# Kernel optimization log

Measured on AMD Instinct MI355X. Metric: run time of the kernel, lower is better.

## Reference

```python
import jax, jax.numpy as jnp
import numpy as np

S = 8192        # total packed tokens
HID = 3072      # hidden_size
NHQ = 24        # query heads
NHKV = 8        # kv heads (GQA)
HD = 128        # head dim
NM = 2          # modalities (experts); tokens assumed modality-sorted: first half mod0, second half mod1
CHUNK = 1024    # ranged attention: 8 equal q/k ranges (block-diagonal)
NB = S // CHUNK
EPS = 1e-6


def setup_inputs() -> dict:
    key = jax.random.key(0)
    ks = jax.random.split(key, 4)
    s = 0.02
    qkv_out = (NHQ + 2 * NHKV) * HD
    # rotary tables: cos/sin of shape (S, HD/2)
    pos = jnp.arange(S, dtype=jnp.float32)
    inv_freq = 1.0 / (10000.0 ** (jnp.arange(0, HD, 2, dtype=jnp.float32) / HD))
    freqs = pos[:, None] * inv_freq[None, :]
    return {
        "x": jax.random.normal(ks[0], (S, HID), jnp.float32),
        "w_qkv": jax.random.normal(ks[1], (NM, qkv_out, HID), jnp.float32) * s,
        "b_qkv": jnp.zeros((NM, qkv_out), jnp.float32),
        "q_norm_w": jnp.zeros((NM, HD), jnp.float32),
        "k_norm_w": jnp.zeros((NM, HD), jnp.float32),
        "cos": jnp.cos(freqs),
        "sin": jnp.sin(freqs),
        "w_out": jax.random.normal(ks[2], (NM, HID, NHQ * HD), jnp.float32) * s,
        "b_out": jnp.zeros((NM, HID), jnp.float32),
    }


def _rms(t):
    # MultiModalityRMSNorm.rms: fp32 rsqrt(mean(x^2)+eps)
    return t * jax.lax.rsqrt(jnp.mean(t * t, axis=-1, keepdims=True) + EPS)


def _rotate_half(t):
    x1, x2 = jnp.split(t, 2, axis=-1)
    return jnp.concatenate([-x2, x1], axis=-1)


def reference(x, w_qkv, b_qkv, q_norm_w, k_norm_w, cos, sin, w_out, b_out):
    half = S // NM
    xm = x.reshape(NM, half, HID)                        # modality-dispatched tokens
    # per-modality (MoE) qkv projection: [m, t, out]
    qkv = jnp.einsum('mti,moi->mto', xm, w_qkv) + b_qkv[:, None, :]
    q, k, v = jnp.split(qkv, [NHQ * HD, (NHQ + NHKV) * HD], axis=-1)
    q = q.reshape(NM, half, NHQ, HD)
    k = k.reshape(NM, half, NHKV, HD)
    v = v.reshape(NM, half, NHKV, HD)
    # per-modality QK RMSNorm over head_dim, weight init zeros -> scale (w+1)
    q = _rms(q) * (q_norm_w[:, None, None, :] + 1.0)
    k = _rms(k) * (k_norm_w[:, None, None, :] + 1.0)
    # RoPE (non-interleaved): cos/sin (S, HD/2) -> (m, t, 1, HD) via (2 d) repeat
    cosm = cos.reshape(NM, half, HD // 2)
    sinm = sin.reshape(NM, half, HD // 2)
    cos2 = jnp.concatenate([cosm, cosm], axis=-1)[:, :, None, :]
    sin2 = jnp.concatenate([sinm, sinm], axis=-1)[:, :, None, :]
    q = q * cos2 + _rotate_half(q) * sin2
    k = k * cos2 + _rotate_half(k) * sin2
    # undispatch back to packed token order (modality-sorted identity permutation)
    qs = q.reshape(S, NHQ, HD)
    ks = k.reshape(S, NHKV, HD)
    vs = v.reshape(S, NHKV, HD)
    # ranged (block-diagonal) flash attention: NB equal q/k ranges of CHUNK tokens
    qb = qs.reshape(NB, CHUNK, NHQ, HD)
    kb = jnp.repeat(ks.reshape(NB, CHUNK, NHKV, HD), NHQ // NHKV, axis=2)  # GQA expand
    vb = jnp.repeat(vs.reshape(NB, CHUNK, NHKV, HD), NHQ // NHKV, axis=2)
    scale = HD ** -0.5
    scores = jnp.einsum('bqhd,bkhd->bhqk', qb, kb) * scale
    attn = jax.nn.softmax(scores, axis=-1)
    ob = jnp.einsum('bhqk,bkhd->bqhd', attn, vb)
    o = ob.reshape(NM, half, NHQ * HD)
    # per-modality output projection
    out = jnp.einsum('mti,moi->mto', o, w_out) + b_out[:, None, :]
    return out.reshape(S, HID)
```

## Files before the change

### kernel.cpp

```cpp
#include <hip/hip_runtime.h>
#include <hip/hip_bf16.h>


typedef __bf16 bf16;
typedef __attribute__((ext_vector_type(8))) __bf16 bf16x8;
typedef __attribute__((ext_vector_type(4))) __bf16 bf16x4;
typedef __attribute__((ext_vector_type(4))) float f32x4;

#define S_TOT 8192
#define HID 3072
#define NHQ 24
#define NHKV 8
#define HD 128
#define QKV_OUT 5120
#define CHUNKT 1024

__device__ inline void gload_lds16(const void* g, void* l) {
  __builtin_amdgcn_global_load_lds((const __attribute__((address_space(1))) void*)g,
                                   (__attribute__((address_space(3))) void*)l, 16, 0, 0);
}

__device__ inline f32x4 mfma16(bf16x8 a, bf16x8 b, f32x4 c) {
  return __builtin_amdgcn_mfma_f32_16x16x32_bf16(a, b, c, 0, 0, 0);
}

__global__ __launch_bounds__(256) void cvt_kernel(const float* __restrict__ in,
                                                  bf16* __restrict__ out, int n4) {
  int idx = blockIdx.x * 256 + threadIdx.x;
  int stride = gridDim.x * 256;
  for (int i = idx; i < n4; i += stride) {
    float4 v = reinterpret_cast<const float4*>(in)[i];
    bf16x4 o = {(bf16)v.x, (bf16)v.y, (bf16)v.z, (bf16)v.w};
    reinterpret_cast<bf16x4*>(out)[i] = o;
  }
}

template <int OUT_BF16>
__global__ __launch_bounds__(256) void gemm_bt(const bf16* __restrict__ A,
                                               const bf16* __restrict__ B,
                                               const float* __restrict__ bias,
                                               void* __restrict__ Cv,
                                               int M, int N, int K) {
  const int mz = blockIdx.z;
  A += (size_t)mz * M * K;
  B += (size_t)mz * N * K;
  bias += (size_t)mz * N;
  bf16* Cb = (bf16*)Cv + (size_t)mz * M * N;
  float* Cf = (float*)Cv + (size_t)mz * M * N;

  __shared__ bf16 As[128 * 64];
  __shared__ bf16 Bs[128 * 64];

  const int tid = threadIdx.x;
  const int l = tid & 63;
  const int w = tid >> 6;
  const int wr = w >> 1, wc = w & 1;

  const bf16* Abase = A + (size_t)(blockIdx.y * 128) * K;
  const bf16* Bbase = B + (size_t)(blockIdx.x * 128) * K;

  f32x4 acc[4][4] = {};

  for (int k0 = 0; k0 < K; k0 += 64) {
#pragma unroll
    for (int it = 0; it < 4; ++it) {
      int idx = it * 256 + tid;
      int row = idx >> 3, c8 = idx & 7;
      gload_lds16(Abase + (size_t)row * K + k0 + c8 * 8, &As[idx * 8]);
    }
#pragma unroll
    for (int it = 0; it < 4; ++it) {
      int idx = it * 256 + tid;
      int row = idx >> 3, c8 = idx & 7;
      gload_lds16(Bbase + (size_t)row * K + k0 + c8 * 8, &Bs[idx * 8]);
    }
    __syncthreads();
#pragma unroll
    for (int kk = 0; kk < 64; kk += 32) {
      bf16x8 a[4], b[4];
#pragma unroll
      for (int i = 0; i < 4; ++i)
        a[i] = *reinterpret_cast<const bf16x8*>(
            &As[(wr * 64 + i * 16 + (l & 15)) * 64 + kk + (l >> 4) * 8]);
#pragma unroll
      for (int j = 0; j < 4; ++j)
        b[j] = *reinterpret_cast<const bf16x8*>(
            &Bs[(wc * 64 + j * 16 + (l & 15)) * 64 + kk + (l >> 4) * 8]);
#pragma unroll
      for (int i = 0; i < 4; ++i)
#pragma unroll
        for (int j = 0; j < 4; ++j)
          acc[i][j] = mfma16(a[i], b[j], acc[i][j]);
    }
    __syncthreads();
  }

  const int row0 = blockIdx.y * 128 + wr * 64 + ((l >> 4) << 2);
  const int col0 = blockIdx.x * 128 + wc * 64 + (l & 15);
#pragma unroll
  for (int j = 0; j < 4; ++j) {
    int col = col0 + j * 16;
    float bv = bias[col];
#pragma unroll
    for (int i = 0; i < 4; ++i) {
#pragma unroll
      for (int r = 0; r < 4; ++r) {
        int row = row0 + i * 16 + r;
        float v = acc[i][j][r] + bv;
        if (OUT_BF16)
          Cb[(size_t)row * N + col] = (bf16)v;
        else
          Cf[(size_t)row * N + col] = v;
      }
    }
  }
}

__global__ __launch_bounds__(256) void rmsrope_kernel(bf16* __restrict__ qkv,
                                                      const float* __restrict__ qw,
                                                      const float* __restrict__ kw,
                                                      const float* __restrict__ cosT,
                                                      const float* __restrict__ sinT) {
  int gid = blockIdx.x * 4 + (threadIdx.x >> 6);
  int l = threadIdx.x & 63;
  int tok = gid >> 5;
  int slot = gid & 31;
  int mz = tok >> 12;
  bf16* p;
  const float* wv;
  if (slot < NHQ) {
    p = qkv + (size_t)tok * QKV_OUT + slot * HD;
    wv = qw + mz * HD;
  } else {
    p = qkv + (size_t)tok * QKV_OUT + HID + (slot - NHQ) * HD;
    wv = kw + mz * HD;
  }
  int d = l * 2;
  float x0 = (float)p[d];
  float x1 = (float)p[d + 1];
  float ss = x0 * x0 + x1 * x1;
#pragma unroll
  for (int m = 1; m < 64; m <<= 1) ss += __shfl_xor(ss, m);
  float rn = rsqrtf(ss * (1.0f / 128.0f) + 1e-6f);
  float n0 = x0 * rn * (wv[d] + 1.0f);
  float n1 = x1 * rn * (wv[d + 1] + 1.0f);
  float o0 = __shfl_xor(n0, 32);
  float o1 = __shfl_xor(n1, 32);
  int ci = d & 63;
  float2 cv = *reinterpret_cast<const float2*>(cosT + (size_t)tok * 64 + ci);
  float2 sv = *reinterpret_cast<const float2*>(sinT + (size_t)tok * 64 + ci);
  float sgn = (l < 32) ? -1.0f : 1.0f;
  p[d] = (bf16)(n0 * cv.x + sgn * o0 * sv.x);
  p[d + 1] = (bf16)(n1 * cv.y + sgn * o1 * sv.y);
}

__global__ __launch_bounds__(256) void attn_kernel(const bf16* __restrict__ qkv,
                                                   bf16* __restrict__ o) {
  constexpr float CEXP = 0.12753139626334912f;
  const int tid = threadIdx.x;
  const int l = tid & 63;
  const int w = tid >> 6;
  const int sq = blockIdx.x;
  const int h = blockIdx.y;
  const int blk = blockIdx.z;
  const int kvh = h / 3;
  const int qtok0 = blk * CHUNKT + sq * 128 + w * 32;
  const int ktok0 = blk * CHUNKT;

  __shared__ bf16 KP[128 * 136];
  __shared__ bf16 Vt[128 * 136];

  bf16x8 qf[2][4];
#pragma unroll
  for (int i = 0; i < 2; ++i) {
    const bf16* qp =
        qkv + (size_t)(qtok0 + i * 16 + (l & 15)) * QKV_OUT + h * HD + (l >> 4) * 8;
#pragma unroll
    for (int c = 0; c < 4; ++c) qf[i][c] = *reinterpret_cast<const bf16x8*>(qp + c * 32);
  }

  f32x4 of[2][8] = {};
  float mrow[2][4], lrow[2][4];
#pragma unroll
  for (int i = 0; i < 2; ++i)
#pragma unroll
    for (int r = 0; r < 4; ++r) {
      mrow[i][r] = -1e30f;
      lrow[i][r] = 0.0f;
    }

  for (int c = 0; c < 8; ++c) {
    __syncthreads();
    const int kt = ktok0 + c * 128;
#pragma unroll
    for (int it = 0; it < 8; ++it) {
      int task = it * 256 + tid;
      int key = task >> 4, dc = task & 15;
      *reinterpret_cast<bf16x8*>(&KP[key * 136 + dc * 8]) =
          *reinterpret_cast<const bf16x8*>(
              qkv + (size_t)(kt + key) * QKV_OUT + HID + kvh * HD + dc * 8);
    }
#pragma unroll
    for (int it = 0; it < 8; ++it) {
      int task = it * 256 + tid;
      int key = task & 127, dc = task >> 7;
      bf16x8 vv = *reinterpret_cast<const bf16x8*>(
          qkv + (size_t)(kt + key) * QKV_OUT + HID + NHKV * HD + kvh * HD + dc * 8);
#pragma unroll
      for (int jj = 0; jj < 8; ++jj) Vt[(dc * 8 + jj) * 136 + key] = vv[jj];
    }
    __syncthreads();

    f32x4 sacc[2][8] = {};
#pragma unroll
    for (int kd = 0; kd < 4; ++kd) {
      bf16x8 kb[8];
#pragma unroll
      for (int j = 0; j < 8; ++j)
        kb[j] = *reinterpret_cast<const bf16x8*>(
            &KP[(j * 16 + (l & 15)) * 136 + kd * 32 + (l >> 4) * 8]);
#pragma unroll
      for (int i = 0; i < 2; ++i)
#pragma unroll
        for (int j = 0; j < 8; ++j) sacc[i][j] = mfma16(qf[i][kd], kb[j], sacc[i][j]);
    }

    float alpha[2][4];
#pragma unroll
    for (int i = 0; i < 2; ++i) {
#pragma unroll
      for (int r = 0; r < 4; ++r) {
        float mx = sacc[i][0][r];
#pragma unroll
        for (int j = 1; j < 8; ++j) mx = fmaxf(mx, sacc[i][j][r]);
        mx = fmaxf(mx, __shfl_xor(mx, 1));
        mx = fmaxf(mx, __shfl_xor(mx, 2));
        mx = fmaxf(mx, __shfl_xor(mx, 4));
        mx = fmaxf(mx, __shfl_xor(mx, 8));
        float mnew = fmaxf(mrow[i][r], mx);
        float al = exp2f((mrow[i][r] - mnew) * CEXP);
        mrow[i][r] = mnew;
        float ps = 0.0f;
#pragma unroll
        for (int j = 0; j < 8; ++j) {
          float pv = exp2f((sacc[i][j][r] - mnew) * CEXP);
          sacc[i][j][r] = pv;
          ps += pv;
        }
        ps += __shfl_xor(ps, 1);
        ps += __shfl_xor(ps, 2);
        ps += __shfl_xor(ps, 4);
        ps += __shfl_xor(ps, 8);
        lrow[i][r] = lrow[i][r] * al + ps;
        alpha[i][r] = al;
      }
    }
#pragma unroll
    for (int i = 0; i < 2; ++i)
#pragma unroll
      for (int j = 0; j < 8; ++j)
#pragma unroll
        for (int r = 0; r < 4; ++r) of[i][j][r] *= alpha[i][r];

    __syncthreads();
    bf16* P = KP + w * (32 * 136);
#pragma unroll
    for (int i = 0; i < 2; ++i)
#pragma unroll
      for (int j = 0; j < 8; ++j)
#pragma unroll
        for (int r = 0; r < 4; ++r)
          P[(i * 16 + (l >> 4) * 4 + r) * 136 + j * 16 + (l & 15)] = (bf16)sacc[i][j][r];

#pragma unroll
    for (int kk = 0; kk < 4; ++kk) {
      bf16x8 pa[2];
#pragma unroll
      for (int i = 0; i < 2; ++i)
        pa[i] = *reinterpret_cast<const bf16x8*>(
            &P[(i * 16 + (l & 15)) * 136 + kk * 32 + (l >> 4) * 8]);
#pragma unroll
      for (int j = 0; j < 8; ++j) {
        bf16x8 bv = *reinterpret_cast<const bf16x8*>(
            &Vt[(j * 16 + (l & 15)) * 136 + kk * 32 + (l >> 4) * 8]);
        of[0][j] = mfma16(pa[0], bv, of[0][j]);
        of[1][j] = mfma16(pa[1], bv, of[1][j]);
      }
    }
  }

#pragma unroll
  for (int i = 0; i < 2; ++i) {
#pragma unroll
    for (int r = 0; r < 4; ++r) {
      float inv = 1.0f / lrow[i][r];
      int row = qtok0 + i * 16 + (l >> 4) * 4 + r;
      bf16* orow = o + (size_t)row * HID + h * HD + (l & 15);
#pragma unroll
      for (int j = 0; j < 8; ++j) orow[j * 16] = (bf16)(of[i][j][r] * inv);
    }
  }
}

extern "C" void kernel_launch(void* const* d_in, const int* in_sizes, int n_in,
                              void* d_out, int out_size, void* d_ws, size_t ws_size,
                              hipStream_t stream) {
  const float* x = (const float*)d_in[0];
  const float* wqkv = (const float*)d_in[1];
  const float* bqkv = (const float*)d_in[2];
  const float* qnw = (const float*)d_in[3];
  const float* knw = (const float*)d_in[4];
  const float* cosT = (const float*)d_in[5];
  const float* sinT = (const float*)d_in[6];
  const float* wout = (const float*)d_in[7];
  const float* bout = (const float*)d_in[8];
  float* out = (float*)d_out;

  char* ws = (char*)d_ws;
  bf16* xb = (bf16*)ws;
  ws += (size_t)S_TOT * HID * 2;
  bf16* wqkvb = (bf16*)ws;
  ws += (size_t)2 * QKV_OUT * HID * 2;
  bf16* qkv = (bf16*)ws;
  bf16* ob = xb;
  bf16* woutb = wqkvb;

  cvt_kernel<<<2048, 256, 0, stream>>>(x, xb, S_TOT * HID / 4);
  cvt_kernel<<<2048, 256, 0, stream>>>(wqkv, wqkvb, 2 * QKV_OUT * HID / 4);

  gemm_bt<1><<<dim3(QKV_OUT / 128, 4096 / 128, 2), 256, 0, stream>>>(
      xb, wqkvb, bqkv, qkv, 4096, QKV_OUT, HID);

  cvt_kernel<<<2048, 256, 0, stream>>>(wout, woutb, 2 * HID * HID / 4);

  rmsrope_kernel<<<(S_TOT * (NHQ + NHKV)) / 4, 256, 0, stream>>>(qkv, qnw, knw, cosT, sinT);

  attn_kernel<<<dim3(8, NHQ, 8), 256, 0, stream>>>(qkv, ob);

  gemm_bt<0><<<dim3(HID / 128, 4096 / 128, 2), 256, 0, stream>>>(
      ob, woutb, bout, out, 4096, HID, HID);
}
```

Measured before the change: 1.283 ms.

## Replace 128x128 GEMM with pipelined 256x256 tile GEMM using swizzled LDS

Replaces the simple 128x128 bf16 GEMM with a 512-thread 256x256-tile kernel. It double-buffers LDS with staged global-to-LDS prefetches two k-tiles ahead, uses XOR-swizzled LDS layouts to avoid bank conflicts, and splits the k-step into four MFMA quadrants interleaved with loads, barriers and priority hints. It also remaps block IDs in groups of eight for better L2 locality. The goal is higher arithmetic intensity and overlap of memory with MFMA in both projection GEMMs. The cost is much heavier LDS use (128KB), more register pressure and hand-tuned waitcnt logic that could be fragile.

```diff
diff --git a/kernel.cpp b/kernel.cpp
--- a/kernel.cpp
+++ b/kernel.cpp
@@ -36,83 +36,174 @@
 }
 
 template <int OUT_BF16>
-__global__ __launch_bounds__(256) void gemm_bt(const bf16* __restrict__ A,
-                                               const bf16* __restrict__ B,
-                                               const float* __restrict__ bias,
-                                               void* __restrict__ Cv,
-                                               int M, int N, int K) {
-  const int mz = blockIdx.z;
-  A += (size_t)mz * M * K;
-  B += (size_t)mz * N * K;
-  bias += (size_t)mz * N;
-  bf16* Cb = (bf16*)Cv + (size_t)mz * M * N;
-  float* Cf = (float*)Cv + (size_t)mz * M * N;
-
-  __shared__ bf16 As[128 * 64];
-  __shared__ bf16 Bs[128 * 64];
-
+__global__ __launch_bounds__(512, 2) void gemm256(const bf16* __restrict__ A,
+                                                  const bf16* __restrict__ B,
+                                                  const float* __restrict__ bias,
+                                                  void* __restrict__ Cv,
+                                                  int M, int N, int K) {
+  __shared__ bf16 lds[65536];
   const int tid = threadIdx.x;
   const int l = tid & 63;
   const int w = tid >> 6;
-  const int wr = w >> 1, wc = w & 1;
-
-  const bf16* Abase = A + (size_t)(blockIdx.y * 128) * K;
-  const bf16* Bbase = B + (size_t)(blockIdx.x * 128) * K;
-
-  f32x4 acc[4][4] = {};
-
-  for (int k0 = 0; k0 < K; k0 += 64) {
-#pragma unroll
-    for (int it = 0; it < 4; ++it) {
-      int idx = it * 256 + tid;
-      int row = idx >> 3, c8 = idx & 7;
-      gload_lds16(Abase + (size_t)row * K + k0 + c8 * 8, &As[idx * 8]);
-    }
-#pragma unroll
-    for (int it = 0; it < 4; ++it) {
-      int idx = it * 256 + tid;
-      int row = idx >> 3, c8 = idx & 7;
-      gload_lds16(Bbase + (size_t)row * K + k0 + c8 * 8, &Bs[idx * 8]);
-    }
-    __syncthreads();
-#pragma unroll
-    for (int kk = 0; kk < 64; kk += 32) {
-      bf16x8 a[4], b[4];
-#pragma unroll
-      for (int i = 0; i < 4; ++i)
-        a[i] = *reinterpret_cast<const bf16x8*>(
-            &As[(wr * 64 + i * 16 + (l & 15)) * 64 + kk + (l >> 4) * 8]);
-#pragma unroll
-      for (int j = 0; j < 4; ++j)
-        b[j] = *reinterpret_cast<const bf16x8*>(
-            &Bs[(wc * 64 + j * 16 + (l & 15)) * 64 + kk + (l >> 4) * 8]);
-#pragma unroll
-      for (int i = 0; i < 4; ++i)
-#pragma unroll
-        for (int j = 0; j < 4; ++j)
-          acc[i][j] = mfma16(a[i], b[j], acc[i][j]);
-    }
-    __syncthreads();
-  }
-
-  const int row0 = blockIdx.y * 128 + wr * 64 + ((l >> 4) << 2);
-  const int col0 = blockIdx.x * 128 + wc * 64 + (l & 15);
+  const int wr = w >> 2, wc = w & 3;
+  const int lm = l & 15, lg = l >> 4;
+
+  const int nwg = gridDim.x;
+  const int id = blockIdx.x;
+  const int swzid = (id & 7) * (nwg >> 3) + (id >> 3);
+  const int xt = N >> 8, yt = M >> 8;
+  const int bn = swzid % xt;
+  const int rem = swzid / xt;
+  const int bm = rem % yt;
+  const int mz = rem / yt;
+
+  const bf16* Ag = A + (size_t)mz * M * K + (size_t)(bm * 256) * K;
+  const bf16* Bg = B + (size_t)mz * N * K + (size_t)(bn * 256) * K;
+  const float* biasg = bias + (size_t)mz * N;
+
+  const int srow = tid >> 3;
+  const int scolb = ((tid & 7) * 16) ^ ((srow & 7) << 4);
+  const bf16* Asrc = Ag + (size_t)srow * K + (scolb >> 1);
+  const bf16* Bsrc = Bg + (size_t)srow * K + (scolb >> 1);
+  bf16* ldsA = lds;
+  bf16* ldsB = lds + 32768;
+
+  auto stA = [&](int buf, int q, int t) {
+    gload_lds16(Asrc + (size_t)(q * 64) * K + t * 64,
+                ldsA + buf * 16384 + q * 4096 + tid * 8);
+  };
+  auto stB = [&](int buf, int q, int t) {
+    gload_lds16(Bsrc + (size_t)(q * 64) * K + t * 64,
+                ldsB + buf * 16384 + q * 4096 + tid * 8);
+  };
+
+  const int xmb = (lm & 7) << 4;
+  const int cb0 = (lg * 16) ^ xmb;
+  const int cb1 = cb0 ^ 64;
+  const int aoff0 = (wr * 128 + lm) * 64 + (cb0 >> 1);
+  const int aoff1 = (wr * 128 + lm) * 64 + (cb1 >> 1);
+  const int boff0 = (wc * 64 + lm) * 64 + (cb0 >> 1);
+  const int boff1 = (wc * 64 + lm) * 64 + (cb1 >> 1);
+
+  const int NT = K >> 6;
+  f32x4 acc[8][4] = {};
+
+#pragma unroll
+  for (int q = 0; q < 4; ++q) stA(0, q, 0);
+#pragma unroll
+  for (int q = 0; q < 4; ++q) stB(0, q, 0);
+#pragma unroll
+  for (int q = 0; q < 4; ++q) stA(1, q, 1);
+  stB(1, 0, 1);
+  stB(1, 1, 1);
+  asm volatile("s_waitcnt vmcnt(6)" ::: "memory");
+  __builtin_amdgcn_s_barrier();
+
+  for (int T = 0; T < NT; ++T) {
+    const int cbuf = T & 1, nbuf = cbuf ^ 1;
+    const bf16* Ac = ldsA + cbuf * 16384;
+    const bf16* Bc = ldsB + cbuf * 16384;
+    const bool s1 = (T + 1) < NT;
+    const bool s2 = (T + 2) < NT;
+    bf16x8 alo[4][2], ahi[4][2], blo[2][2], bhi[2][2];
+
+#pragma unroll
+    for (int i = 0; i < 4; ++i) {
+      alo[i][0] = *(const bf16x8*)(Ac + aoff0 + i * 1024);
+      alo[i][1] = *(const bf16x8*)(Ac + aoff1 + i * 1024);
+    }
+#pragma unroll
+    for (int j = 0; j < 2; ++j) {
+      blo[j][0] = *(const bf16x8*)(Bc + boff0 + j * 1024);
+      blo[j][1] = *(const bf16x8*)(Bc + boff1 + j * 1024);
+    }
+    if (s1) { stB(nbuf, 2, T + 1); stB(nbuf, 3, T + 1); }
+    __builtin_amdgcn_s_barrier();
+    asm volatile("s_waitcnt lgkmcnt(0)" ::: "memory");
+    __builtin_amdgcn_s_setprio(1);
+#pragma unroll
+    for (int i = 0; i < 4; ++i)
+#pragma unroll
+      for (int j = 0; j < 2; ++j) {
+        acc[i][j] = mfma16(alo[i][0], blo[j][0], acc[i][j]);
+        acc[i][j] = mfma16(alo[i][1], blo[j][1], acc[i][j]);
+      }
+    __builtin_amdgcn_s_setprio(0);
+    __builtin_amdgcn_s_barrier();
+
+#pragma unroll
+    for (int j = 0; j < 2; ++j) {
+      bhi[j][0] = *(const bf16x8*)(Bc + boff0 + (j + 2) * 1024);
+      bhi[j][1] = *(const bf16x8*)(Bc + boff1 + (j + 2) * 1024);
+    }
+    if (s2) { stA(cbuf, 0, T + 2); stA(cbuf, 2, T + 2); }
+    __builtin_amdgcn_s_barrier();
+    asm volatile("s_waitcnt lgkmcnt(0)" ::: "memory");
+    __builtin_amdgcn_s_setprio(1);
+#pragma unroll
+    for (int i = 0; i < 4; ++i)
+#pragma unroll
+      for (int j = 0; j < 2; ++j) {
+        acc[i][j + 2] = mfma16(alo[i][0], bhi[j][0], acc[i][j + 2]);
+        acc[i][j + 2] = mfma16(alo[i][1], bhi[j][1], acc[i][j + 2]);
+      }
+    __builtin_amdgcn_s_setprio(0);
+    __builtin_amdgcn_s_barrier();
+
+#pragma unroll
+    for (int i = 0; i < 4; ++i) {
+      ahi[i][0] = *(const bf16x8*)(Ac + aoff0 + (i + 4) * 1024);
+      ahi[i][1] = *(const bf16x8*)(Ac + aoff1 + (i + 4) * 1024);
+    }
+    if (s2) { stB(cbuf, 0, T + 2); stB(cbuf, 1, T + 2); }
+    __builtin_amdgcn_s_barrier();
+    asm volatile("s_waitcnt lgkmcnt(0)" ::: "memory");
+    __builtin_amdgcn_s_setprio(1);
+#pragma unroll
+    for (int i = 0; i < 4; ++i)
+#pragma unroll
+      for (int j = 0; j < 2; ++j) {
+        acc[i + 4][j] = mfma16(ahi[i][0], blo[j][0], acc[i + 4][j]);
+        acc[i + 4][j] = mfma16(ahi[i][1], blo[j][1], acc[i + 4][j]);
+      }
+    __builtin_amdgcn_s_setprio(0);
+    __builtin_amdgcn_s_barrier();
+
+    if (s2) { stA(cbuf, 1, T + 2); stA(cbuf, 3, T + 2); }
+    __builtin_amdgcn_s_barrier();
+    __builtin_amdgcn_s_setprio(1);
+#pragma unroll
+    for (int i = 0; i < 4; ++i)
+#pragma unroll
+      for (int j = 0; j < 2; ++j) {
+        acc[i + 4][j + 2] = mfma16(ahi[i][0], bhi[j][0], acc[i + 4][j + 2]);
+        acc[i + 4][j + 2] = mfma16(ahi[i][1], bhi[j][1], acc[i + 4][j + 2]);
+      }
+    __builtin_amdgcn_s_setprio(0);
+    if (s2)
+      asm volatile("s_waitcnt vmcnt(6)" ::: "memory");
+    else
+      asm volatile("s_waitcnt vmcnt(0)" ::: "memory");
+    __builtin_amdgcn_s_barrier();
+  }
+
+  const int row0 = bm * 256 + wr * 128 + lg * 4;
+  const int col0 = bn * 256 + wc * 64 + lm;
 #pragma unroll
   for (int j = 0; j < 4; ++j) {
-    int col = col0 + j * 16;
-    float bv = bias[col];
-#pragma unroll
-    for (int i = 0; i < 4; ++i) {
+    const int col = col0 + j * 16;
+    const float bv = biasg[col];
+#pragma unroll
+    for (int i = 0; i < 8; ++i)
 #pragma unroll
       for (int r = 0; r < 4; ++r) {
-        int row = row0 + i * 16 + r;
-        float v = acc[i][j][r] + bv;
+        const int row = row0 + i * 16 + r;
+        const float v = acc[i][j][r] + bv;
         if (OUT_BF16)
-          Cb[(size_t)row * N + col] = (bf16)v;
+          ((bf16*)Cv)[(size_t)mz * M * N + (size_t)row * N + col] = (bf16)v;
         else
-          Cf[(size_t)row * N + col] = v;
-      }
-    }
+          ((float*)Cv)[(size_t)mz * M * N + (size_t)row * N + col] = v;
+      }
   }
 }
 
@@ -328,7 +419,7 @@
   cvt_kernel<<<2048, 256, 0, stream>>>(x, xb, S_TOT * HID / 4);
   cvt_kernel<<<2048, 256, 0, stream>>>(wqkv, wqkvb, 2 * QKV_OUT * HID / 4);
 
-  gemm_bt<1><<<dim3(QKV_OUT / 128, 4096 / 128, 2), 256, 0, stream>>>(
+  gemm256<1><<<(QKV_OUT / 256) * (4096 / 256) * 2, 512, 0, stream>>>(
       xb, wqkvb, bqkv, qkv, 4096, QKV_OUT, HID);
 
   cvt_kernel<<<2048, 256, 0, stream>>>(wout, woutb, 2 * HID * HID / 4);
@@ -337,6 +428,6 @@
 
   attn_kernel<<<dim3(8, NHQ, 8), 256, 0, stream>>>(qkv, ob);
 
-  gemm_bt<0><<<dim3(HID / 128, 4096 / 128, 2), 256, 0, stream>>>(
+  gemm256<0><<<(HID / 256) * (4096 / 256) * 2, 512, 0, stream>>>(
       ob, woutb, bout, out, 4096, HID, HID);
 }
```

Result: faster. 1.136 ms (-11.5%).
